# Kernel optimization log

Measured on AMD Instinct MI355X. Metric: run time of the kernel, lower is better.

The kernel has to match this reference:

```python
import jax, jax.numpy as jnp
import numpy as np

N = 30000      # num nodes (cells)
E = 480000     # num edges (avg degree 16)
D_IN = 1000    # input_dim (genes)
H = 8          # nheads
F_H = 32       # hidden_dim per head
D_EMB = 64     # embedding_dim
NEG_SLOPE = 0.2


def setup_inputs() -> dict:
    key = jax.random.key(0)
    ks = jax.random.split(key, 12)
    glorot = lambda k, shape, fan: (jax.random.normal(k, shape, jnp.float32)
                                    * (1.0 / np.sqrt(fan)))
    return {
        "x": jax.random.normal(ks[0], (N, D_IN), jnp.float32),
        "edge_index": jax.random.randint(ks[1], (2, E), 0, N),
        "edge_weight": jax.random.uniform(ks[2], (E,), jnp.float32),
        # GATConv params
        "W": glorot(ks[3], (D_IN, H * F_H), D_IN),
        "att_src": glorot(ks[4], (H, F_H), F_H),
        "att_dst": glorot(ks[5], (H, F_H), F_H),
        "bias_gat": jnp.zeros((H * F_H,), jnp.float32),
        # embedding Linear
        "emb_W": glorot(ks[6], (H * F_H, D_EMB), H * F_H),
        "emb_b": jnp.zeros((D_EMB,), jnp.float32),
        # decoder MLP
        "dec_W1": glorot(ks[7], (D_EMB, F_H), D_EMB),
        "dec_b1": jnp.zeros((F_H,), jnp.float32),
        "dec_W2": glorot(ks[8], (F_H, D_IN), F_H),
        "dec_b2": jnp.zeros((D_IN,), jnp.float32),
    }


def _gat_conv(x, edge_index, W, att_src, att_dst, bias):
    n = x.shape[0]
    h = (x @ W).reshape(n, H, F_H)                    # [N,H,F]
    a_s = jnp.einsum('nhf,hf->nh', h, att_src)        # [N,H]
    a_d = jnp.einsum('nhf,hf->nh', h, att_dst)        # [N,H]
    # add self loops (PyG default add_self_loops=True)
    loops = jnp.arange(n)
    src = jnp.concatenate([edge_index[0], loops])     # [E+N]
    dst = jnp.concatenate([edge_index[1], loops])     # [E+N]
    logits = jax.nn.leaky_relu(a_s[src] + a_d[dst], NEG_SLOPE)  # [E+N,H]
    # segment softmax over incoming edges of each destination node
    m = jax.ops.segment_max(logits, dst, num_segments=n)        # [N,H]
    p = jnp.exp(logits - m[dst])
    denom = jax.ops.segment_sum(p, dst, num_segments=n)         # [N,H]
    alpha = p / denom[dst]                                      # [E+N,H]
    msg = h[src] * alpha[:, :, None]                            # [E+N,H,F]
    out = jax.ops.segment_sum(msg, dst, num_segments=n)         # [N,H,F]
    return out.reshape(n, H * F_H) + bias


def reference(x, edge_index, edge_weight, W, att_src, att_dst, bias_gat,
              emb_W, emb_b, dec_W1, dec_b1, dec_W2, dec_b2):
    # edge_weight is accepted but unused: PyG GATConv with edge_dim=None has
    # no edge-feature pathway.
    h = jax.nn.relu(_gat_conv(x, edge_index, W, att_src, att_dst, bias_gat))
    z = h @ emb_W + emb_b                               # [N, D_EMB]
    d = jax.nn.relu(z @ dec_W1 + dec_b1)                # [N, F_H]
    recon = d @ dec_W2 + dec_b2                         # [N, D_IN]
    return recon, z
```

## Files before the change

### kernel.cpp

```cpp
#include <hip/hip_runtime.h>
#include <hip/hip_bf16.h>

#define N_NODES 30000
#define N_EDGES 480000
#define D_IN    1000
#define KPAD    1024
#define NHEAD   8
#define F_HID   32
#define D_EMB   64
#define NEG_SLOPE 0.2f
#define MAXDEG  64

typedef __attribute__((ext_vector_type(4))) float  f32x4;
typedef __attribute__((ext_vector_type(8))) __bf16 bf16x8;
typedef __attribute__((ext_vector_type(4))) __bf16 bf16x4;

#define XB_BLOCKS 15000
#define WT_TOT    (256*KPAD + D_EMB*256 + F_HID*D_EMB + D_IN*F_HID)
#define WT_BLOCKS ((WT_TOT + 255) / 256)
#define ZC_BLOCKS ((N_NODES + 255) / 256)

__global__ __launch_bounds__(256) void cvt_all(
    const float* __restrict__ x, const float* __restrict__ W,
    const float* __restrict__ emb_W, const float* __restrict__ d1,
    const float* __restrict__ d2,
    __bf16* __restrict__ xb, __bf16* __restrict__ WbT,
    __bf16* __restrict__ embT, __bf16* __restrict__ d1T,
    __bf16* __restrict__ d2T, int* __restrict__ cnt)
{
    int b = blockIdx.x;
    if (b < XB_BLOCKS) {
        int i = b * 256 + threadIdx.x;
        int row = i >> 7;
        int col = (i & 127) * 8;
        bf16x8 o;
        if (col < D_IN) {
            const f32x4* p = (const f32x4*)(x + (size_t)row * D_IN + col);
            f32x4 a = p[0], bb = p[1];
            o[0]=(__bf16)a.x;  o[1]=(__bf16)a.y;  o[2]=(__bf16)a.z;  o[3]=(__bf16)a.w;
            o[4]=(__bf16)bb.x; o[5]=(__bf16)bb.y; o[6]=(__bf16)bb.z; o[7]=(__bf16)bb.w;
        } else {
            #pragma unroll
            for (int j = 0; j < 8; j++) o[j] = (__bf16)0.0f;
        }
        *(bf16x8*)(xb + (size_t)row * KPAD + col) = o;
        return;
    }
    b -= XB_BLOCKS;
    if (b < WT_BLOCKS) {
        int i = b * 256 + threadIdx.x;
        if (i < 256 * KPAD) {
            int n = i >> 10, k = i & 1023;
            WbT[i] = (k < D_IN) ? (__bf16)W[(size_t)k * 256 + n] : (__bf16)0.0f;
            return;
        }
        i -= 256 * KPAD;
        if (i < D_EMB * 256) {
            int n = i >> 8, k = i & 255;
            embT[i] = (__bf16)emb_W[(size_t)k * D_EMB + n];
            return;
        }
        i -= D_EMB * 256;
        if (i < F_HID * D_EMB) {
            int n = i >> 6, k = i & 63;
            d1T[i] = (__bf16)d1[(size_t)k * F_HID + n];
            return;
        }
        i -= F_HID * D_EMB;
        if (i < D_IN * F_HID) {
            int n = i >> 5, k = i & 31;
            d2T[i] = (__bf16)d2[(size_t)k * D_IN + n];
        }
        return;
    }
    b -= WT_BLOCKS;
    {
        int i = b * 256 + threadIdx.x;
        if (i < N_NODES) cnt[i] = 0;
    }
}

__device__ __forceinline__ void stage_tile(
    __bf16* lds, const __bf16* __restrict__ g, int base, int maxr,
    int K, int k0, int rows, int w, int lane)
{
    const int rsub = lane >> 2;
    const int c    = lane & 3;
    for (int off = w * 1024; off < rows * 64; off += 4096) {
        int r  = (off >> 6) + rsub;
        int gr = base + r; gr = gr > maxr ? maxr : gr;
        int chunk = c ^ (r & 3);
        const __bf16* gp = g + (size_t)gr * K + k0 + chunk * 8;
        __builtin_amdgcn_global_load_lds(
            (const __attribute__((address_space(1))) void*)gp,
            (__attribute__((address_space(3))) void*)((char*)lds + off),
            16, 0, 0);
    }
}

template<int BM, int BN, int RELU>
__global__ __launch_bounds__(256) void gemm_bf16(
    const __bf16* __restrict__ A, const __bf16* __restrict__ Bt,
    float* __restrict__ Cf, __bf16* __restrict__ Cb,
    const float* __restrict__ bias, int M, int Nn, int K)
{
    constexpr int MT = BM / 32;
    constexpr int NT = BN / 32;
    __shared__ __align__(16) __bf16 As[BM * 32];
    __shared__ __align__(16) __bf16 Bs[BN * 32];

    const int tid  = threadIdx.x;
    const int w    = tid >> 6, lane = tid & 63;
    const int wm   = w >> 1,   wn   = w & 1;
    const int quad = lane >> 4, l16 = lane & 15;
    const int bm = blockIdx.x * BM, bn = blockIdx.y * BN;

    f32x4 acc[MT][NT];
    #pragma unroll
    for (int i = 0; i < MT; i++)
        #pragma unroll
        for (int j = 0; j < NT; j++)
            acc[i][j] = (f32x4){0.f, 0.f, 0.f, 0.f};

    for (int k0 = 0; k0 < K; k0 += 32) {
        stage_tile(As, A,  bm, M  - 1, K, k0, BM, w, lane);
        stage_tile(Bs, Bt, bn, Nn - 1, K, k0, BN, w, lane);
        __syncthreads();

        bf16x8 af[MT], bfr[NT];
        #pragma unroll
        for (int mt = 0; mt < MT; mt++) {
            int r = wm * 64 + mt * 16 + l16;
            af[mt] = *(const bf16x8*)&As[r * 32 + (quad ^ (r & 3)) * 8];
        }
        #pragma unroll
        for (int nt = 0; nt < NT; nt++) {
            int r = wn * (NT * 16) + nt * 16 + l16;
            bfr[nt] = *(const bf16x8*)&Bs[r * 32 + (quad ^ (r & 3)) * 8];
        }
        #pragma unroll
        for (int mt = 0; mt < MT; mt++)
            #pragma unroll
            for (int nt = 0; nt < NT; nt++)
                acc[mt][nt] = __builtin_amdgcn_mfma_f32_16x16x32_bf16(
                    af[mt], bfr[nt], acc[mt][nt], 0, 0, 0);
        __syncthreads();
    }

    #pragma unroll
    for (int nt = 0; nt < NT; nt++) {
        int col = bn + wn * (NT * 16) + nt * 16 + l16;
        if (col >= Nn) continue;
        float bv = bias ? bias[col] : 0.0f;
        #pragma unroll
        for (int mt = 0; mt < MT; mt++) {
            int row0 = bm + wm * 64 + mt * 16 + quad * 4;
            #pragma unroll
            for (int rr = 0; rr < 4; rr++) {
                int row = row0 + rr;
                if (row < M) {
                    float v = acc[mt][nt][rr] + bv;
                    if (RELU) v = v > 0.f ? v : 0.f;
                    if (Cf) Cf[(size_t)row * Nn + col] = v;
                    if (Cb) Cb[(size_t)row * Nn + col] = (__bf16)v;
                }
            }
        }
    }
}

#define ATT_BLOCKS ((N_NODES * NHEAD + 255) / 256)
#define SC_BLOCKS  ((N_EDGES + 255) / 256)

__global__ __launch_bounds__(256) void att_scatter(
    const __bf16* __restrict__ hb, const float* __restrict__ att_src,
    const float* __restrict__ att_dst, const int* __restrict__ eidx,
    float* __restrict__ a_s, float* __restrict__ a_d,
    int* __restrict__ cnt, int* __restrict__ slots)
{
    int b = blockIdx.x;
    if (b < ATT_BLOCKS) {
        int i = b * 256 + threadIdx.x;
        if (i >= N_NODES * NHEAD) return;
        int hh = i & 7;
        const bf16x8* hp = (const bf16x8*)(hb + (size_t)i * F_HID);
        const float* sp = att_src + hh * F_HID;
        const float* dp = att_dst + hh * F_HID;
        float s = 0.f, d = 0.f;
        #pragma unroll
        for (int j = 0; j < 4; j++) {
            bf16x8 hv = hp[j];
            #pragma unroll
            for (int t = 0; t < 8; t++) {
                float f = (float)hv[t];
                s += f * sp[j * 8 + t];
                d += f * dp[j * 8 + t];
            }
        }
        a_s[i] = s;
        a_d[i] = d;
        return;
    }
    b -= ATT_BLOCKS;
    {
        int e = b * 256 + threadIdx.x;
        if (e < N_EDGES) {
            int d = eidx[N_EDGES + e];
            int slot = atomicAdd(&cnt[d], 1);
            slots[d * MAXDEG + slot] = eidx[e];
        }
    }
}

__device__ __forceinline__ float leaky(float x) {
    return x > 0.f ? x : NEG_SLOPE * x;
}

__global__ __launch_bounds__(256) void gat_aggregate(
    const __bf16* __restrict__ hb, const float* __restrict__ a_s,
    const float* __restrict__ a_d, const int* __restrict__ cnt,
    const int* __restrict__ slots, const float* __restrict__ bias,
    __bf16* __restrict__ hgatb)
{
    const int wid  = threadIdx.x >> 6;
    const int lane = threadIdx.x & 63;
    const int n = blockIdx.x * 4 + wid;
    if (n >= N_NODES) return;

    const int hh = lane >> 3;
    const int fo = (lane & 7) * 4;
    const int base = n * MAXDEG;
    const int c = cnt[n];
    const float adn = a_d[n * NHEAD + hh];

    float p = __expf(leaky(a_s[n * NHEAD + hh] + adn));
    float denom = p;
    f32x4 acc;
    {
        bf16x4 hv = *(const bf16x4*)(hb + (size_t)n * 256 + hh * F_HID + fo);
        acc.x = p * (float)hv[0]; acc.y = p * (float)hv[1];
        acc.z = p * (float)hv[2]; acc.w = p * (float)hv[3];
    }
    int e = 0;
    for (; e + 4 <= c; e += 4) {
        int s0 = slots[base + e + 0];
        int s1 = slots[base + e + 1];
        int s2 = slots[base + e + 2];
        int s3 = slots[base + e + 3];
        float l0 = a_s[s0 * NHEAD + hh], l1 = a_s[s1 * NHEAD + hh];
        float l2 = a_s[s2 * NHEAD + hh], l3 = a_s[s3 * NHEAD + hh];
        bf16x4 h0 = *(const bf16x4*)(hb + (size_t)s0 * 256 + hh * F_HID + fo);
        bf16x4 h1 = *(const bf16x4*)(hb + (size_t)s1 * 256 + hh * F_HID + fo);
        bf16x4 h2 = *(const bf16x4*)(hb + (size_t)s2 * 256 + hh * F_HID + fo);
        bf16x4 h3 = *(const bf16x4*)(hb + (size_t)s3 * 256 + hh * F_HID + fo);
        float p0 = __expf(leaky(l0 + adn)), p1 = __expf(leaky(l1 + adn));
        float p2 = __expf(leaky(l2 + adn)), p3 = __expf(leaky(l3 + adn));
        denom += (p0 + p1) + (p2 + p3);
        acc.x += p0*(float)h0[0] + p1*(float)h1[0] + p2*(float)h2[0] + p3*(float)h3[0];
        acc.y += p0*(float)h0[1] + p1*(float)h1[1] + p2*(float)h2[1] + p3*(float)h3[1];
        acc.z += p0*(float)h0[2] + p1*(float)h1[2] + p2*(float)h2[2] + p3*(float)h3[2];
        acc.w += p0*(float)h0[3] + p1*(float)h1[3] + p2*(float)h2[3] + p3*(float)h3[3];
    }
    for (; e < c; e++) {
        int s = slots[base + e];
        float pe = __expf(leaky(a_s[s * NHEAD + hh] + adn));
        denom += pe;
        bf16x4 hv = *(const bf16x4*)(hb + (size_t)s * 256 + hh * F_HID + fo);
        acc.x += pe * (float)hv[0]; acc.y += pe * (float)hv[1];
        acc.z += pe * (float)hv[2]; acc.w += pe * (float)hv[3];
    }
    float inv = 1.0f / denom;
    f32x4 bv = *(const f32x4*)(bias + lane * 4);
    float o0 = acc.x * inv + bv.x, o1 = acc.y * inv + bv.y;
    float o2 = acc.z * inv + bv.z, o3 = acc.w * inv + bv.w;
    o0 = o0 > 0.f ? o0 : 0.f;
    o1 = o1 > 0.f ? o1 : 0.f;
    o2 = o2 > 0.f ? o2 : 0.f;
    o3 = o3 > 0.f ? o3 : 0.f;
    bf16x4 ob;
    ob[0] = (__bf16)o0; ob[1] = (__bf16)o1; ob[2] = (__bf16)o2; ob[3] = (__bf16)o3;
    *(bf16x4*)(hgatb + (size_t)n * 256 + lane * 4) = ob;
}

__global__ __launch_bounds__(256) void gemm_zd(
    const __bf16* __restrict__ hgatb, const __bf16* __restrict__ embT,
    const __bf16* __restrict__ d1T, const float* __restrict__ emb_b,
    const float* __restrict__ dec_b1, float* __restrict__ z,
    __bf16* __restrict__ dbufb, int M)
{
    __shared__ __align__(16) __bf16 As[128 * 32];
    __shared__ __align__(16) __bf16 Bs[64 * 32];
    __shared__ __align__(16) __bf16 zS[128 * 64];
    __shared__ __align__(16) __bf16 Bs2[2 * 32 * 32];

    const int tid  = threadIdx.x;
    const int w    = tid >> 6, lane = tid & 63;
    const int wm   = w >> 1,   wn   = w & 1;
    const int quad = lane >> 4, l16 = lane & 15;
    const int bm = blockIdx.x * 128;

    stage_tile(Bs2,        d1T, 0, 31, 64, 0,  32, w, lane);
    stage_tile(Bs2 + 1024, d1T, 0, 31, 64, 32, 32, w, lane);

    f32x4 acc[4][2];
    #pragma unroll
    for (int i = 0; i < 4; i++) { acc[i][0] = (f32x4){0,0,0,0}; acc[i][1] = (f32x4){0,0,0,0}; }

    for (int k0 = 0; k0 < 256; k0 += 32) {
        stage_tile(As, hgatb, bm, M - 1, 256, k0, 128, w, lane);
        stage_tile(Bs, embT,  0,  D_EMB - 1, 256, k0, 64, w, lane);
        __syncthreads();
        bf16x8 af[4], bfr[2];
        #pragma unroll
        for (int mt = 0; mt < 4; mt++) {
            int r = wm * 64 + mt * 16 + l16;
            af[mt] = *(const bf16x8*)&As[r * 32 + (quad ^ (r & 3)) * 8];
        }
        #pragma unroll
        for (int nt = 0; nt < 2; nt++) {
            int r = wn * 32 + nt * 16 + l16;
            bfr[nt] = *(const bf16x8*)&Bs[r * 32 + (quad ^ (r & 3)) * 8];
        }
        #pragma unroll
        for (int mt = 0; mt < 4; mt++)
            #pragma unroll
            for (int nt = 0; nt < 2; nt++)
                acc[mt][nt] = __builtin_amdgcn_mfma_f32_16x16x32_bf16(
                    af[mt], bfr[nt], acc[mt][nt], 0, 0, 0);
        __syncthreads();
    }

    #pragma unroll
    for (int nt = 0; nt < 2; nt++) {
        int col = wn * 32 + nt * 16 + l16;
        float bv = emb_b[col];
        int t = col >> 5, cch = (col >> 3) & 3, j = col & 7;
        #pragma unroll
        for (int mt = 0; mt < 4; mt++) {
            int rl0 = wm * 64 + mt * 16 + quad * 4;
            #pragma unroll
            for (int rr = 0; rr < 4; rr++) {
                int rl = rl0 + rr;
                int row = bm + rl;
                float v = acc[mt][nt][rr] + bv;
                if (row < M) z[(size_t)row * D_EMB + col] = v;
                zS[t * 4096 + rl * 32 + (cch ^ (rl & 3)) * 8 + j] = (__bf16)v;
            }
        }
    }
    __syncthreads();

    f32x4 accd[4];
    #pragma unroll
    for (int i = 0; i < 4; i++) accd[i] = (f32x4){0,0,0,0};
    #pragma unroll
    for (int t = 0; t < 2; t++) {
        bf16x8 af[4], bfr;
        #pragma unroll
        for (int mt = 0; mt < 4; mt++) {
            int r = wm * 64 + mt * 16 + l16;
            af[mt] = *(const bf16x8*)&zS[t * 4096 + r * 32 + (quad ^ (r & 3)) * 8];
        }
        {
            int r = wn * 16 + l16;
            bfr = *(const bf16x8*)&Bs2[t * 1024 + r * 32 + (quad ^ (r & 3)) * 8];
        }
        #pragma unroll
        for (int mt = 0; mt < 4; mt++)
            accd[mt] = __builtin_amdgcn_mfma_f32_16x16x32_bf16(af[mt], bfr, accd[mt], 0, 0, 0);
    }
    {
        int col = wn * 16 + l16;
        float bv = dec_b1[col];
        #pragma unroll
        for (int mt = 0; mt < 4; mt++) {
            int rl0 = wm * 64 + mt * 16 + quad * 4;
            #pragma unroll
            for (int rr = 0; rr < 4; rr++) {
                int row = bm + rl0 + rr;
                if (row < M) {
                    float v = accd[mt][rr] + bv;
                    v = v > 0.f ? v : 0.f;
                    dbufb[(size_t)row * F_HID + col] = (__bf16)v;
                }
            }
        }
    }
}

extern "C" void kernel_launch(void* const* d_in, const int* in_sizes, int n_in,
                              void* d_out, int out_size, void* d_ws, size_t ws_size,
                              hipStream_t stream)
{
    const float* x        = (const float*)d_in[0];
    const int*   eidx     = (const int*)  d_in[1];
    const float* W        = (const float*)d_in[3];
    const float* att_src  = (const float*)d_in[4];
    const float* att_dst  = (const float*)d_in[5];
    const float* bias_gat = (const float*)d_in[6];
    const float* emb_W    = (const float*)d_in[7];
    const float* emb_b    = (const float*)d_in[8];
    const float* dec_W1   = (const float*)d_in[9];
    const float* dec_b1   = (const float*)d_in[10];
    const float* dec_W2   = (const float*)d_in[11];
    const float* dec_b2   = (const float*)d_in[12];

    float* out   = (float*)d_out;
    float* recon = out;
    float* z     = out + (size_t)N_NODES * D_IN;

    __bf16* xb = (__bf16*)recon;

    char* ws = (char*)d_ws;
    size_t o = 0;
    auto alloc = [&](size_t bytes) { char* p = ws + o; o = (o + bytes + 255) & ~(size_t)255; return p; };
    __bf16* hb      = (__bf16*)alloc((size_t)N_NODES * 256 * 2);
    __bf16* WbT     = (__bf16*)alloc((size_t)256 * KPAD * 2);
    __bf16* embT    = (__bf16*)alloc((size_t)D_EMB * 256 * 2);
    __bf16* d1T     = (__bf16*)alloc((size_t)F_HID * D_EMB * 2);
    __bf16* d2T     = (__bf16*)alloc((size_t)D_IN * F_HID * 2);
    __bf16* hgatb   = (__bf16*)alloc((size_t)N_NODES * 256 * 2);
    __bf16* dbufb   = (__bf16*)alloc((size_t)N_NODES * F_HID * 2);
    float*  a_s     = (float*) alloc((size_t)N_NODES * NHEAD * 4);
    float*  a_d     = (float*) alloc((size_t)N_NODES * NHEAD * 4);
    int*    slots   = (int*)   alloc((size_t)N_NODES * MAXDEG * 4);
    int*    cnt     = (int*)   alloc((size_t)N_NODES * 4);

    const int MB = (N_NODES + 127) / 128;

    cvt_all<<<XB_BLOCKS + WT_BLOCKS + ZC_BLOCKS, 256, 0, stream>>>(
        x, W, emb_W, dec_W1, dec_W2, xb, WbT, embT, d1T, d2T, cnt);

    gemm_bf16<128, 128, 0><<<dim3(MB, 2), 256, 0, stream>>>(
        xb, WbT, (float*)nullptr, hb, (const float*)nullptr, N_NODES, 256, KPAD);

    att_scatter<<<ATT_BLOCKS + SC_BLOCKS, 256, 0, stream>>>(
        hb, att_src, att_dst, eidx, a_s, a_d, cnt, slots);

    gat_aggregate<<<N_NODES / 4, 256, 0, stream>>>(
        hb, a_s, a_d, cnt, slots, bias_gat, hgatb);

    gemm_zd<<<MB, 256, 0, stream>>>(
        hgatb, embT, d1T, emb_b, dec_b1, z, dbufb, N_NODES);

    gemm_bf16<128, 128, 0><<<dim3(MB, 8), 256, 0, stream>>>(
        dbufb, d2T, recon, (__bf16*)nullptr, dec_b2, N_NODES, D_IN, F_HID);
}
```

Before: 415.9 us.

## Fuse fp32-to-bf16 conversion of x into first GEMM with full-N tile

Drops the separate pass that converted x to a padded bf16 buffer. The first GEMM now loads fp32 rows directly, converts them in registers and writes a swizzled LDS tile, prefetching the next K-slice. Each block covers all 256 output columns, so x is read once instead of once per column tile, and the bf16 round trip through global memory goes away. In exchange, occupancy drops to one large-accumulator block per CU and the grid shrinks to about 235 blocks.

```diff
diff --git a/kernel.cpp b/kernel.cpp
--- a/kernel.cpp
+++ b/kernel.cpp
@@ -15,38 +15,17 @@
 typedef __attribute__((ext_vector_type(8))) __bf16 bf16x8;
 typedef __attribute__((ext_vector_type(4))) __bf16 bf16x4;
 
-#define XB_BLOCKS 15000
 #define WT_TOT    (256*KPAD + D_EMB*256 + F_HID*D_EMB + D_IN*F_HID)
 #define WT_BLOCKS ((WT_TOT + 255) / 256)
 #define ZC_BLOCKS ((N_NODES + 255) / 256)
 
-__global__ __launch_bounds__(256) void cvt_all(
-    const float* __restrict__ x, const float* __restrict__ W,
-    const float* __restrict__ emb_W, const float* __restrict__ d1,
-    const float* __restrict__ d2,
-    __bf16* __restrict__ xb, __bf16* __restrict__ WbT,
-    __bf16* __restrict__ embT, __bf16* __restrict__ d1T,
-    __bf16* __restrict__ d2T, int* __restrict__ cnt)
+__global__ __launch_bounds__(256) void cvt_w(
+    const float* __restrict__ W, const float* __restrict__ emb_W,
+    const float* __restrict__ d1, const float* __restrict__ d2,
+    __bf16* __restrict__ WbT, __bf16* __restrict__ embT,
+    __bf16* __restrict__ d1T, __bf16* __restrict__ d2T, int* __restrict__ cnt)
 {
     int b = blockIdx.x;
-    if (b < XB_BLOCKS) {
-        int i = b * 256 + threadIdx.x;
-        int row = i >> 7;
-        int col = (i & 127) * 8;
-        bf16x8 o;
-        if (col < D_IN) {
-            const f32x4* p = (const f32x4*)(x + (size_t)row * D_IN + col);
-            f32x4 a = p[0], bb = p[1];
-            o[0]=(__bf16)a.x;  o[1]=(__bf16)a.y;  o[2]=(__bf16)a.z;  o[3]=(__bf16)a.w;
-            o[4]=(__bf16)bb.x; o[5]=(__bf16)bb.y; o[6]=(__bf16)bb.z; o[7]=(__bf16)bb.w;
-        } else {
-            #pragma unroll
-            for (int j = 0; j < 8; j++) o[j] = (__bf16)0.0f;
-        }
-        *(bf16x8*)(xb + (size_t)row * KPAD + col) = o;
-        return;
-    }
-    b -= XB_BLOCKS;
     if (b < WT_BLOCKS) {
         int i = b * 256 + threadIdx.x;
         if (i < 256 * KPAD) {
@@ -164,6 +143,101 @@
                     if (Cf) Cf[(size_t)row * Nn + col] = v;
                     if (Cb) Cb[(size_t)row * Nn + col] = (__bf16)v;
                 }
+            }
+        }
+    }
+}
+
+__device__ __forceinline__ void a_load_f32(
+    const float* __restrict__ x, int bm, int M, int r0, int cb, f32x4* regs)
+{
+    if (cb < D_IN) {
+        int g0 = bm + r0;      g0 = g0 > M - 1 ? M - 1 : g0;
+        int g1 = bm + r0 + 64; g1 = g1 > M - 1 ? M - 1 : g1;
+        const f32x4* p0 = (const f32x4*)(x + (size_t)g0 * D_IN + cb);
+        const f32x4* p1 = (const f32x4*)(x + (size_t)g1 * D_IN + cb);
+        regs[0] = p0[0]; regs[1] = p0[1];
+        regs[2] = p1[0]; regs[3] = p1[1];
+    } else {
+        regs[0] = regs[1] = regs[2] = regs[3] = (f32x4){0.f, 0.f, 0.f, 0.f};
+    }
+}
+
+__global__ __launch_bounds__(256, 1) void gemm1_fused(
+    const float* __restrict__ x, const __bf16* __restrict__ WbT,
+    __bf16* __restrict__ hb, int M)
+{
+    __shared__ __align__(16) __bf16 As[128 * 32];
+    __shared__ __align__(16) __bf16 Bs[256 * 32];
+
+    const int tid  = threadIdx.x;
+    const int w    = tid >> 6, lane = tid & 63;
+    const int wm   = w >> 1,   wn   = w & 1;
+    const int quad = lane >> 4, l16 = lane & 15;
+    const int bm   = blockIdx.x * 128;
+
+    const int r0   = tid >> 2;
+    const int cpos = tid & 3;
+    const int cxor = (cpos ^ (r0 & 3)) << 3;
+
+    f32x4 acc[4][8];
+    #pragma unroll
+    for (int i = 0; i < 4; i++)
+        #pragma unroll
+        for (int j = 0; j < 8; j++)
+            acc[i][j] = (f32x4){0.f, 0.f, 0.f, 0.f};
+
+    f32x4 ca[4], na[4];
+    a_load_f32(x, bm, M, r0, cxor, ca);
+
+    for (int k0 = 0; k0 < KPAD; k0 += 32) {
+        a_load_f32(x, bm, M, r0, (k0 + 32) + cxor, na);
+        stage_tile(Bs, WbT, 0, 255, KPAD, k0, 256, w, lane);
+        {
+            bf16x8 o;
+            o[0]=(__bf16)ca[0].x; o[1]=(__bf16)ca[0].y; o[2]=(__bf16)ca[0].z; o[3]=(__bf16)ca[0].w;
+            o[4]=(__bf16)ca[1].x; o[5]=(__bf16)ca[1].y; o[6]=(__bf16)ca[1].z; o[7]=(__bf16)ca[1].w;
+            *(bf16x8*)&As[r0 * 32 + cpos * 8] = o;
+            o[0]=(__bf16)ca[2].x; o[1]=(__bf16)ca[2].y; o[2]=(__bf16)ca[2].z; o[3]=(__bf16)ca[2].w;
+            o[4]=(__bf16)ca[3].x; o[5]=(__bf16)ca[3].y; o[6]=(__bf16)ca[3].z; o[7]=(__bf16)ca[3].w;
+            *(bf16x8*)&As[(r0 + 64) * 32 + cpos * 8] = o;
+        }
+        __syncthreads();
+
+        bf16x8 af[4], bfr[8];
+        #pragma unroll
+        for (int mt = 0; mt < 4; mt++) {
+            int r = wm * 64 + mt * 16 + l16;
+            af[mt] = *(const bf16x8*)&As[r * 32 + (quad ^ (r & 3)) * 8];
+        }
+        #pragma unroll
+        for (int nt = 0; nt < 8; nt++) {
+            int r = wn * 128 + nt * 16 + l16;
+            bfr[nt] = *(const bf16x8*)&Bs[r * 32 + (quad ^ (r & 3)) * 8];
+        }
+        #pragma unroll
+        for (int mt = 0; mt < 4; mt++)
+            #pragma unroll
+            for (int nt = 0; nt < 8; nt++)
+                acc[mt][nt] = __builtin_amdgcn_mfma_f32_16x16x32_bf16(
+                    af[mt], bfr[nt], acc[mt][nt], 0, 0, 0);
+        __syncthreads();
+
+        #pragma unroll
+        for (int i = 0; i < 4; i++) ca[i] = na[i];
+    }
+
+    #pragma unroll
+    for (int nt = 0; nt < 8; nt++) {
+        int col = wn * 128 + nt * 16 + l16;
+        #pragma unroll
+        for (int mt = 0; mt < 4; mt++) {
+            int row0 = bm + wm * 64 + mt * 16 + quad * 4;
+            #pragma unroll
+            for (int rr = 0; rr < 4; rr++) {
+                int row = row0 + rr;
+                if (row < M)
+                    hb[(size_t)row * 256 + col] = (__bf16)acc[mt][nt][rr];
             }
         }
     }
@@ -409,8 +483,6 @@
     float* recon = out;
     float* z     = out + (size_t)N_NODES * D_IN;
 
-    __bf16* xb = (__bf16*)recon;
-
     char* ws = (char*)d_ws;
     size_t o = 0;
     auto alloc = [&](size_t bytes) { char* p = ws + o; o = (o + bytes + 255) & ~(size_t)255; return p; };
@@ -428,11 +500,10 @@
 
     const int MB = (N_NODES + 127) / 128;
 
-    cvt_all<<<XB_BLOCKS + WT_BLOCKS + ZC_BLOCKS, 256, 0, stream>>>(
-        x, W, emb_W, dec_W1, dec_W2, xb, WbT, embT, d1T, d2T, cnt);
-
-    gemm_bf16<128, 128, 0><<<dim3(MB, 2), 256, 0, stream>>>(
-        xb, WbT, (float*)nullptr, hb, (const float*)nullptr, N_NODES, 256, KPAD);
+    cvt_w<<<WT_BLOCKS + ZC_BLOCKS, 256, 0, stream>>>(
+        W, emb_W, dec_W1, dec_W2, WbT, embT, d1T, d2T, cnt);
+
+    gemm1_fused<<<MB, 256, 0, stream>>>(x, WbT, hb, N_NODES);
 
     att_scatter<<<ATT_BLOCKS + SC_BLOCKS, 256, 0, stream>>>(
         hb, att_src, att_dst, eidx, a_s, a_d, cnt, slots);
```

After: 419.7 us. Within noise of the previous version (+0.9%).
